# Optimization experiments

Hardware: AMD Instinct MI355X
Metric: run time of the kernel (lower is better)

Reference implementation:

```python
import jax, jax.numpy as jnp
import numpy as np

H = 48; W = 48; C_IN = 32; C_OUT = 64
L = 4                      # liftsamples
RADIUS = 3                 # neighborhood radius
CMCO = 16                  # LieConv PointConv fixed mid channels
FOCAL = W / np.pi          # equidistant fisheye focal
CX, CY = (W - 1) / 2.0, (H - 1) / 2.0
EPS = 1e-7


def _build_neighbor_indices(h, w, radius):
    offs = [(dx, dy) for dy in range(-radius, radius + 1)
            for dx in range(-radius, radius + 1)
            if dx * dx + dy * dy <= radius * radius]
    offs = np.array(offs, dtype=np.int64)  # (k,2) as (dx,dy)
    yy, xx = np.meshgrid(np.arange(h), np.arange(w), indexing='ij')
    yy = yy.reshape(-1, 1); xx = xx.reshape(-1, 1)
    ny = yy + offs[None, :, 1]; nx = xx + offs[None, :, 0]
    valid = (ny >= 0) & (ny < h) & (nx >= 0) & (nx < w)
    idx = ny * w + nx
    return np.where(valid, idx, -1).astype(np.int32)  # (h*w, k)


def swish(x):
    return x * jax.nn.sigmoid(x)


def so3_exp(wvec):
    # Rodrigues: (...,3) -> (...,3,3)
    th = jnp.maximum(jnp.linalg.norm(wvec, axis=-1, keepdims=True), EPS)
    k = wvec / th
    kx, ky, kz = k[..., 0], k[..., 1], k[..., 2]
    z = jnp.zeros_like(kx)
    K = jnp.stack([jnp.stack([z, -kz, ky], -1),
                   jnp.stack([kz, z, -kx], -1),
                   jnp.stack([-ky, kx, z], -1)], -2)
    th = th[..., None]
    I = jnp.eye(3, dtype=wvec.dtype)
    return I + jnp.sin(th) * K + (1.0 - jnp.cos(th)) * (K @ K)


def so3_log(R):
    # (...,3,3) -> (...,3)
    tr = R[..., 0, 0] + R[..., 1, 1] + R[..., 2, 2]
    cos = jnp.clip((tr - 1.0) * 0.5, -1.0 + 1e-6, 1.0 - 1e-6)
    th = jnp.arccos(cos)
    v = jnp.stack([R[..., 2, 1] - R[..., 1, 2],
                   R[..., 0, 2] - R[..., 2, 0],
                   R[..., 1, 0] - R[..., 0, 1]], -1)
    return v * (th / (2.0 * jnp.sin(th)))[..., None]


def setup_inputs() -> dict:
    key = jax.random.key(0)
    ks = jax.random.split(key, 6)
    def lin(k, fi, fo):
        return jax.random.normal(k, (fi, fo), jnp.float32) / np.sqrt(fi)
    return {
        'x': jax.random.normal(ks[0], (2, C_IN, H, W), jnp.float32),
        'neighbor_idx': jnp.asarray(_build_neighbor_indices(H, W, RADIUS)),
        'W1': lin(ks[1], 3, 32), 'b1': jnp.zeros((32,), jnp.float32),
        'W2': lin(ks[2], 32, 32), 'b2': jnp.zeros((32,), jnp.float32),
        'W3': lin(ks[3], 32, CMCO), 'b3': jnp.zeros((CMCO,), jnp.float32),
        'Wl': lin(ks[4], CMCO * C_IN, C_OUT), 'bl': jnp.zeros((C_OUT,), jnp.float32),
    }


def _lift_log(dtype):
    # pixel grid -> unit rays -> so(3) log of lifted group elems, shape (n*L, 3)
    u = jnp.arange(W, dtype=dtype); v = jnp.arange(H, dtype=dtype)
    uu, vv = jnp.meshgrid(u, v)               # 'xy' indexing, (H,W)
    dx = (uu - CX).reshape(-1); dy = (vv - CY).reshape(-1)
    r = jnp.sqrt(dx * dx + dy * dy)
    theta = r / FOCAL
    rs = jnp.maximum(r, EPS)
    rays = jnp.stack([jnp.sin(theta) * dx / rs,
                      jnp.sin(theta) * dy / rs,
                      jnp.cos(theta)], -1)    # (n,3)
    pz = jnp.clip(rays[:, 2], -1.0 + 1e-6, 1.0 - 1e-6)
    ang = jnp.arccos(pz)
    axis = jnp.stack([-rays[:, 1], rays[:, 0], jnp.zeros_like(pz)], -1)
    axis = axis / jnp.maximum(jnp.linalg.norm(axis, axis=-1, keepdims=True), EPS)
    Rp = so3_exp(axis * ang[:, None])          # (n,3,3), Rp @ e3 = ray
    alphas = jnp.arange(L, dtype=dtype) * (2.0 * np.pi / L)
    Rz = so3_exp(jnp.stack([jnp.zeros_like(alphas), jnp.zeros_like(alphas), alphas], -1))
    Rlift = jnp.einsum('nij,ljk->nlik', Rp, Rz)  # (n,L,3,3)
    return so3_log(Rlift).reshape(H * W * L, 3)


def reference(x, neighbor_idx, W1, b1, W2, b2, W3, b3, Wl, bl):
    bs, c, h, w = x.shape
    n = h * w
    k = neighbor_idx.shape[1]
    nL, K = n * L, k * L

    a = _lift_log(x.dtype)                                   # (nL,3)

    valid = neighbor_idx >= 0                                # (n,k)
    safe_pix = jnp.maximum(neighbor_idx, 0).astype(jnp.int32)
    # lifted neighbor indices: query lift copy l sees all (j, l') neighbors
    nb_lift = safe_pix[:, None, :, None] * L + jnp.arange(L, dtype=jnp.int32)[None, None, None, :]
    nb_lift = jnp.broadcast_to(nb_lift, (n, L, k, L)).reshape(nL, K)
    nb_pix = jnp.broadcast_to(safe_pix[:, None, :, None], (n, L, k, L)).reshape(nL, K)
    mask = jnp.broadcast_to(valid[:, None, :, None], (n, L, k, L)).reshape(nL, K)

    # pairwise group elements: log(exp(-b) @ exp(a))
    b_log = a[nb_lift]                                       # (nL,K,3)
    Rab = jnp.einsum('qmij,qjk->qmik', so3_exp(-b_log), so3_exp(a))
    ab = so3_log(Rab)                                        # (nL,K,3)

    # kernel MLP (WeightNet: 3 -> 32 -> 32 -> 16, swish)
    hdn = swish(ab @ W1 + b1)
    hdn = swish(hdn @ W2 + b2)
    wts = swish(hdn @ W3 + b3)                               # (nL,K,16)
    wts = jnp.where(mask[..., None], wts, 0.0)

    values = x.transpose(0, 2, 3, 1).reshape(bs, n, c)       # (bs,n,c)
    nv = values[:, nb_pix]                                   # (bs,nL,K,c)
    partial = jnp.einsum('bqmc,qmf->bqcf', nv, wts).reshape(bs, nL, c * CMCO)
    out = partial @ Wl + bl                                  # (bs,nL,c_out)
    out = out.reshape(bs, n, L, -1).mean(axis=2)             # pool over lift samples
    return out.reshape(bs, h, w, -1).transpose(0, 3, 1, 2)   # (bs,c_out,h,w)
```

## Files before the change

kernel.cpp:

```cpp
#include <hip/hip_runtime.h>

#define WW   48
#define NPIX 2304
#define CIN  32
#define COUT 64
#define KNB  29
#define FCO  16
#define NPJ  (NPIX * KNB)
#define GEN_WAVES  ((NPJ + 6) / 7)
#define GEN_BLOCKS ((GEN_WAVES + 3) / 4)

#define WS_RP64 0
#define WS_EAB  165888
#define WS_EG   248832
#define WS_M0   1133568
#define WS_V    1133632
#define WS_PART 4340800

__device__ __forceinline__ float swish_f(float x) {
    return x * __builtin_amdgcn_rcpf(1.0f + __expf(-x));
}

__device__ __forceinline__ void so3_exp_d(double wx, double wy, double wz, double R[9]) {
    double n  = sqrt(wx * wx + wy * wy + wz * wz);
    double th = fmax(n, 1e-7);
    double kx = wx / th, ky = wy / th, kz = wz / th;
    double s = sin(th), c = cos(th);
    double omc = 1.0 - c;
    R[0] = 1.0 + omc * (kx * kx - 1.0);
    R[1] = -s * kz + omc * kx * ky;
    R[2] =  s * ky + omc * kx * kz;
    R[3] =  s * kz + omc * kx * ky;
    R[4] = 1.0 + omc * (ky * ky - 1.0);
    R[5] = -s * kx + omc * ky * kz;
    R[6] = -s * ky + omc * kz * kx;
    R[7] =  s * kx + omc * kz * ky;
    R[8] = 1.0 + omc * (kz * kz - 1.0);
}

__device__ __forceinline__ void compute_Rp_d(int p, double R[9]) {
    int ui = p % WW, vi = p / WW;
    double dx = (double)ui - 23.5;
    double dy = (double)vi - 23.5;
    double r  = sqrt(dx * dx + dy * dy);
    const double FOCAL = 48.0 / 3.14159265358979323846;
    double theta = r / FOCAL;
    double rs = fmax(r, 1e-7);
    double st = sin(theta);
    double rayx = st * dx / rs;
    double rayy = st * dy / rs;
    double rayz = cos(theta);
    double pz  = fmin(fmax(rayz, -1.0 + 1e-6), 1.0 - 1e-6);
    double ang = acos(pz);
    double ax = -rayy, ay = rayx;
    double an = fmax(sqrt(ax * ax + ay * ay), 1e-7);
    ax /= an; ay /= an;
    so3_exp_d(ax * ang, ay * ang, 0.0, R);
}

__device__ __forceinline__ void mlp_half(float ab0, float ab1, float ab2, const int Q0,
    const float* __restrict__ W1, const float* __restrict__ b1,
    const float* __restrict__ W2, const float* __restrict__ b2,
    const float* __restrict__ W3, const float* __restrict__ b3,
    float* acc3) {
    float accq[16];
    #pragma unroll
    for (int q = 0; q < 16; ++q) accq[q] = b2[Q0 + q];
    #pragma unroll
    for (int i = 0; i < 32; ++i) {
        float h = swish_f(b1[i] + ab0 * W1[i] + ab1 * W1[32 + i] + ab2 * W1[64 + i]);
        #pragma unroll
        for (int q = 0; q < 16; ++q) accq[q] += h * W2[i * 32 + Q0 + q];
    }
    #pragma unroll
    for (int q = 0; q < 16; ++q) {
        float h2 = swish_f(accq[q]);
        #pragma unroll
        for (int f = 0; f < FCO; ++f) acc3[f] += h2 * W3[(Q0 + q) * FCO + f];
    }
}

__device__ __forceinline__ void mlp_eval(float ab0, float ab1, float ab2,
    const float* __restrict__ W1, const float* __restrict__ b1,
    const float* __restrict__ W2, const float* __restrict__ b2,
    const float* __restrict__ W3, const float* __restrict__ b3,
    float* o) {
    float acc3[FCO];
    #pragma unroll
    for (int f = 0; f < FCO; ++f) acc3[f] = b3[f];
    mlp_half(ab0, ab1, ab2, 0,  W1, b1, W2, b2, W3, b3, acc3);
    __builtin_amdgcn_sched_barrier(0);
    mlp_half(ab0, ab1, ab2, 16, W1, b1, W2, b2, W3, b3, acc3);
    #pragma unroll
    for (int f = 0; f < FCO; ++f) o[f] = swish_f(acc3[f]);
}

__global__ __launch_bounds__(256)
void rp_kernel(double* __restrict__ rp64, float* __restrict__ eab) {
    int p = blockIdx.x * 256 + threadIdx.x;
    if (p >= NPIX) return;
    double R[9];
    compute_Rp_d(p, R);
    #pragma unroll
    for (int e = 0; e < 9; ++e) rp64[p * 9 + e] = R[e];
    #pragma unroll
    for (int m = 0; m < 3; ++m) {
        int l = m + (m >> 1);
        double c = (l == 0) ? 1.0 : 0.0;
        double s = (l == 1) ? 1.0 : ((l == 3) ? -1.0 : 0.0);
        double M[9];
        #pragma unroll
        for (int i = 0; i < 3; ++i) {
            M[i * 3 + 0] =  R[i * 3 + 0] * c + R[i * 3 + 1] * s;
            M[i * 3 + 1] = -R[i * 3 + 0] * s + R[i * 3 + 1] * c;
            M[i * 3 + 2] =  R[i * 3 + 2];
        }
        double tr   = M[0] + M[4] + M[8];
        double cosv = fmin(fmax((tr - 1.0) * 0.5, -1.0 + 1e-6), 1.0 - 1e-6);
        double th   = acos(cosv);
        double sv   = sqrt((1.0 - cosv) * (1.0 + cosv));
        double fac  = th / (2.0 * sv);
        eab[p * 9 + m * 3 + 0] = (float)((M[7] - M[5]) * fac);
        eab[p * 9 + m * 3 + 1] = (float)((M[2] - M[6]) * fac);
        eab[p * 9 + m * 3 + 2] = (float)((M[3] - M[1]) * fac);
    }
}

__global__ __launch_bounds__(256)
void vlog2_kernel(const int* __restrict__ nbr, const double* __restrict__ rp64,
                  float* __restrict__ vws) {
    int tid = blockIdx.x * 256 + threadIdx.x;
    if (tid >= NPJ * 4) return;
    int g2 = tid >> 2;
    int d  = tid & 3;
    int p = g2 / KNB, j = g2 - p * KNB;
    int pj = max(nbr[p * KNB + j], 0);
    double Rq[9];
    #pragma unroll
    for (int q = 0; q < 9; ++q) Rq[q] = rp64[p * 9 + q];
    double X[9];
    #pragma unroll
    for (int q = 0; q < 9; ++q) X[q] = 0.0;
    #pragma unroll
    for (int k = 0; k < 3; ++k) {
        double rn0 = rp64[pj * 9 + k * 3 + 0];
        double rn1 = rp64[pj * 9 + k * 3 + 1];
        double rn2 = rp64[pj * 9 + k * 3 + 2];
        #pragma unroll
        for (int jj = 0; jj < 3; ++jj) {
            X[0 * 3 + jj] += rn0 * Rq[k * 3 + jj];
            X[1 * 3 + jj] += rn1 * Rq[k * 3 + jj];
            X[2 * 3 + jj] += rn2 * Rq[k * 3 + jj];
        }
    }
    double c = (d == 0) ? 1.0 : ((d == 2) ? -1.0 : 0.0);
    double s = (d == 1) ? 1.0 : ((d == 3) ? -1.0 : 0.0);
    double M0 =  X[0] * c + X[1] * s;
    double M1 = -X[0] * s + X[1] * c;
    double M2 =  X[2];
    double M3 =  X[3] * c + X[4] * s;
    double M4 = -X[3] * s + X[4] * c;
    double M5 =  X[5];
    double M6 =  X[6] * c + X[7] * s;
    double M7 = -X[6] * s + X[7] * c;
    double M8 =  X[8];
    double tr   = M0 + M4 + M8;
    double cosv = fmin(fmax((tr - 1.0) * 0.5, -1.0 + 1e-6), 1.0 - 1e-6);
    double th   = acos(cosv);
    double svv  = sqrt((1.0 - cosv) * (1.0 + cosv));
    double fac  = th / (2.0 * svv);
    float* dst = vws + g2 * 12 + d * 3;
    dst[0] = (float)((M7 - M5) * fac);
    dst[1] = (float)((M2 - M6) * fac);
    dst[2] = (float)((M3 - M1) * fac);
}

__global__ __launch_bounds__(256)
void edge_kernel(const float* __restrict__ W1, const float* __restrict__ b1,
                 const float* __restrict__ W2, const float* __restrict__ b2,
                 const float* __restrict__ W3, const float* __restrict__ b3,
                 const float* __restrict__ eab,
                 float* __restrict__ eg, float* __restrict__ m0v) {
    int g = blockIdx.x * 256 + threadIdx.x;
    if (g > NPIX * 6) return;
    bool isz = (g == NPIX * 6);
    int gc = isz ? 0 : g;
    int pix = gc / 6, which = gc - pix * 6;
    int m = (which < 3) ? which : (which - 3);
    float sg = isz ? 0.f : ((which < 3) ? 1.f : -1.f);
    const float* ep = eab + pix * 9 + m * 3;
    float o[FCO];
    mlp_eval(sg * ep[0], sg * ep[1], sg * ep[2], W1, b1, W2, b2, W3, b3, o);
    float* dst = isz ? m0v : (eg + g * FCO);
    #pragma unroll
    for (int f = 0; f < FCO; ++f) dst[f] = o[f];
}

__global__ __launch_bounds__(256)
void mlp1_kernel(const float* __restrict__ W1, const float* __restrict__ b1,
                 const float* __restrict__ W2, const float* __restrict__ b2,
                 const float* __restrict__ W3, const float* __restrict__ b3,
                 const float* __restrict__ vws, float* __restrict__ part) {
    int wave = blockIdx.x * 4 + (threadIdx.x >> 6);
    int lane = threadIdx.x & 63;
    int slot = lane / 9;
    int e    = lane - slot * 9;
    int g2   = wave * 7 + slot;
    int g2c  = min(g2, NPJ - 1);
    int l1m = e / 3, l2m = e - l1m * 3;
    int l1 = l1m + (l1m >> 1);
    int l2 = l2m + (l2m >> 1);
    int d  = (l1 - l2) & 3;
    const float* vp = vws + g2c * 12 + d * 3;
    float v0 = vp[0], v1 = vp[1], v2 = vp[2];
    float ab0 = (l2m == 0) ? v0 : ((l2m == 1) ?  v1 : -v1);
    float ab1 = (l2m == 0) ? v1 : ((l2m == 1) ? -v0 :  v0);
    float o[FCO];
    mlp_eval(ab0, ab1, v2, W1, b1, W2, b2, W3, b3, o);
    #pragma unroll
    for (int f = 0; f < FCO; ++f) {
        float a = o[f];
        a += __shfl(a, min(lane + 1, 63)) + __shfl(a, min(lane + 2, 63));
        a += __shfl(a, min(lane + 3, 63)) + __shfl(a, min(lane + 6, 63));
        o[f] = a;
    }
    if (e == 0 && lane < 63 && g2 < NPJ) {
        float* dst = part + g2 * FCO;
        #pragma unroll
        for (int f = 0; f < FCO; ++f) dst[f] = o[f];
    }
}

__global__ __launch_bounds__(256)
void agg_kernel(const float* __restrict__ x, const int* __restrict__ nbr,
                const float* __restrict__ Wl, const float* __restrict__ bl,
                const float* __restrict__ eg, const float* __restrict__ m0v,
                const float* __restrict__ part, float* __restrict__ out) {
    __shared__ int   spj[KNB];
    __shared__ int   sval[KNB];
    __shared__ float sE[FCO];
    __shared__ float sS[KNB][FCO];
    __shared__ float sxv[2][CIN][KNB];
    __shared__ float sT[2][CIN][FCO];
    __shared__ float spp[256];

    const int p = blockIdx.x;
    const int t = threadIdx.x;

    if (t < KNB) {
        int idx = nbr[p * KNB + t];
        spj[t]  = max(idx, 0);
        sval[t] = (idx >= 0) ? 1 : 0;
    } else if (t >= 32 && t < 32 + FCO) {
        int f = t - 32;
        sE[f] = eg[(p * 6 + 0) * FCO + f] + eg[(p * 6 + 1) * FCO + f]
              + eg[(p * 6 + 2) * FCO + f] + m0v[f];
    }
    __syncthreads();

    for (int e = t; e < 2 * CIN * KNB; e += 256) {
        int bb = e / (CIN * KNB);
        int r  = e - bb * (CIN * KNB);
        int c  = r / KNB;
        int j  = r - c * KNB;
        sxv[bb][c][j] = x[bb * (CIN * NPIX) + c * NPIX + spj[j]];
    }
    for (int idx = t; idx < KNB * FCO; idx += 256) {
        int j = idx >> 4, f = idx & 15;
        float acc = part[(p * KNB + j) * FCO + f];
        int n6 = spj[j] * 6;
        acc += eg[(n6 + 3) * FCO + f] + eg[(n6 + 4) * FCO + f] + eg[(n6 + 5) * FCO + f];
        acc += sE[f];
        sS[j][f] = sval[j] ? acc * 0.25f : 0.f;
    }
    __syncthreads();

    for (int tt = t; tt < 2 * CIN * FCO; tt += 256) {
        int bb = tt >> 9;
        int c  = (tt >> 4) & 31;
        int f  = tt & 15;
        float acc = 0.f;
        #pragma unroll
        for (int j = 0; j < KNB; ++j)
            acc += sxv[bb][c][j] * sS[j][f];
        sT[bb][c][f] = acc;
    }
    __syncthreads();

    {
        int half = t >> 7, q = t & 127, bb = q >> 6, co = q & 63;
        const float* Tb = &sT[bb][0][0];
        float acc = 0.f;
        int cf0 = half * 256;
        #pragma unroll 8
        for (int cf = cf0; cf < cf0 + 256; ++cf)
            acc += Tb[cf] * Wl[cf * COUT + co];
        spp[t] = acc;
    }
    __syncthreads();
    if (t < 128) {
        int bb = t >> 6, co = t & 63;
        out[bb * (COUT * NPIX) + co * NPIX + p] = spp[t] + spp[t + 128] + bl[co];
    }
}

extern "C" void kernel_launch(void* const* d_in, const int* in_sizes, int n_in,
                              void* d_out, int out_size, void* d_ws, size_t ws_size,
                              hipStream_t stream) {
    const float* x  = (const float*)d_in[0];
    const int* nbr  = (const int*)d_in[1];
    const float* W1 = (const float*)d_in[2];
    const float* b1 = (const float*)d_in[3];
    const float* W2 = (const float*)d_in[4];
    const float* b2 = (const float*)d_in[5];
    const float* W3 = (const float*)d_in[6];
    const float* b3 = (const float*)d_in[7];
    const float* Wl = (const float*)d_in[8];
    const float* bl = (const float*)d_in[9];
    float* out = (float*)d_out;

    char* ws = (char*)d_ws;
    double* rp64 = (double*)(ws + WS_RP64);
    float*  eab  = (float*)(ws + WS_EAB);
    float*  eg   = (float*)(ws + WS_EG);
    float*  m0v  = (float*)(ws + WS_M0);
    float*  vws  = (float*)(ws + WS_V);
    float*  part = (float*)(ws + WS_PART);

    hipLaunchKernelGGL(rp_kernel, dim3((NPIX + 255) / 256), dim3(256), 0, stream,
                       rp64, eab);
    hipLaunchKernelGGL(vlog2_kernel, dim3((NPJ * 4 + 255) / 256), dim3(256), 0, stream,
                       nbr, rp64, vws);
    hipLaunchKernelGGL(edge_kernel, dim3((NPIX * 6 + 1 + 255) / 256), dim3(256), 0, stream,
                       W1, b1, W2, b2, W3, b3, eab, eg, m0v);
    hipLaunchKernelGGL(mlp1_kernel, dim3(GEN_BLOCKS), dim3(256), 0, stream,
                       W1, b1, W2, b2, W3, b3, vws, part);
    hipLaunchKernelGGL(agg_kernel, dim3(NPIX), dim3(256), 0, stream,
                       x, nbr, Wl, bl, eg, m0v, part, out);
}
```

Measured before the change: 94.74 us.

## Split rp and edge MLP work across four threads and share Wl loads

rp_kernel now uses four threads per pixel, one writing the rotation and three computing the lifted logs, so more threads are in flight. edge_kernel splits each edge's MLP hidden layer across four lanes and combines the partial third-layer sums with xor shuffles, which cuts per-thread serial work and register pressure. In agg_kernel's final projection, 128 threads each load a Wl element once and apply it to both batches instead of 256 threads loading it separately. The cost is redundant compute of the pixel rotation and first layer in each lane, plus extra shuffles.

After: 86.29 us. 1.1x faster.

```diff
diff --git a/kernel.cpp b/kernel.cpp
--- a/kernel.cpp
+++ b/kernel.cpp
@@ -9,6 +9,7 @@
 #define NPJ  (NPIX * KNB)
 #define GEN_WAVES  ((NPJ + 6) / 7)
 #define GEN_BLOCKS ((GEN_WAVES + 3) / 4)
+#define NEDGE (NPIX * 6 + 1)
 
 #define WS_RP64 0
 #define WS_EAB  165888
@@ -97,14 +98,16 @@
 
 __global__ __launch_bounds__(256)
 void rp_kernel(double* __restrict__ rp64, float* __restrict__ eab) {
-    int p = blockIdx.x * 256 + threadIdx.x;
-    if (p >= NPIX) return;
+    int tid = blockIdx.x * 256 + threadIdx.x;
+    if (tid >= NPIX * 4) return;
+    int p = tid >> 2, which = tid & 3;
     double R[9];
     compute_Rp_d(p, R);
-    #pragma unroll
-    for (int e = 0; e < 9; ++e) rp64[p * 9 + e] = R[e];
-    #pragma unroll
-    for (int m = 0; m < 3; ++m) {
+    if (which == 0) {
+        #pragma unroll
+        for (int e = 0; e < 9; ++e) rp64[p * 9 + e] = R[e];
+    } else {
+        int m = which - 1;
         int l = m + (m >> 1);
         double c = (l == 0) ? 1.0 : 0.0;
         double s = (l == 1) ? 1.0 : ((l == 3) ? -1.0 : 0.0);
@@ -181,19 +184,48 @@
                  const float* __restrict__ W3, const float* __restrict__ b3,
                  const float* __restrict__ eab,
                  float* __restrict__ eg, float* __restrict__ m0v) {
-    int g = blockIdx.x * 256 + threadIdx.x;
-    if (g > NPIX * 6) return;
+    int tid = blockIdx.x * 256 + threadIdx.x;
+    int g  = tid >> 2;
+    int ql = tid & 3;
+    if (g >= NEDGE) return;
     bool isz = (g == NPIX * 6);
     int gc = isz ? 0 : g;
     int pix = gc / 6, which = gc - pix * 6;
     int m = (which < 3) ? which : (which - 3);
     float sg = isz ? 0.f : ((which < 3) ? 1.f : -1.f);
     const float* ep = eab + pix * 9 + m * 3;
-    float o[FCO];
-    mlp_eval(sg * ep[0], sg * ep[1], sg * ep[2], W1, b1, W2, b2, W3, b3, o);
-    float* dst = isz ? m0v : (eg + g * FCO);
-    #pragma unroll
-    for (int f = 0; f < FCO; ++f) dst[f] = o[f];
+    float ab0 = sg * ep[0], ab1 = sg * ep[1], ab2 = sg * ep[2];
+    const int Q0 = ql * 8;
+    float accq[8];
+    #pragma unroll
+    for (int q = 0; q < 8; ++q) accq[q] = b2[Q0 + q];
+    #pragma unroll
+    for (int i = 0; i < 32; ++i) {
+        float h = swish_f(b1[i] + ab0 * W1[i] + ab1 * W1[32 + i] + ab2 * W1[64 + i]);
+        #pragma unroll
+        for (int q = 0; q < 8; ++q) accq[q] += h * W2[i * 32 + Q0 + q];
+    }
+    float part3[FCO];
+    #pragma unroll
+    for (int f = 0; f < FCO; ++f) part3[f] = 0.f;
+    #pragma unroll
+    for (int q = 0; q < 8; ++q) {
+        float h2 = swish_f(accq[q]);
+        #pragma unroll
+        for (int f = 0; f < FCO; ++f) part3[f] += h2 * W3[(Q0 + q) * FCO + f];
+    }
+    #pragma unroll
+    for (int f = 0; f < FCO; ++f) {
+        float a = part3[f];
+        a += __shfl_xor(a, 1);
+        a += __shfl_xor(a, 2);
+        part3[f] = a;
+    }
+    if (ql == 0) {
+        float* dst = isz ? m0v : (eg + g * FCO);
+        #pragma unroll
+        for (int f = 0; f < FCO; ++f) dst[f] = swish_f(b3[f] + part3[f]);
+    }
 }
 
 __global__ __launch_bounds__(256)
@@ -287,20 +319,26 @@
     }
     __syncthreads();
 
-    {
-        int half = t >> 7, q = t & 127, bb = q >> 6, co = q & 63;
-        const float* Tb = &sT[bb][0][0];
-        float acc = 0.f;
+    if (t < 128) {
+        int half = t >> 6, co = t & 63;
+        const float* Tb0 = &sT[0][0][0];
+        const float* Tb1 = &sT[1][0][0];
+        float a0 = 0.f, a1 = 0.f;
         int cf0 = half * 256;
         #pragma unroll 8
-        for (int cf = cf0; cf < cf0 + 256; ++cf)
-            acc += Tb[cf] * Wl[cf * COUT + co];
-        spp[t] = acc;
+        for (int cf = cf0; cf < cf0 + 256; ++cf) {
+            float w = Wl[cf * COUT + co];
+            a0 += Tb0[cf] * w;
+            a1 += Tb1[cf] * w;
+        }
+        spp[half * 128 + 0 * 64 + co] = a0;
+        spp[half * 128 + 1 * 64 + co] = a1;
     }
     __syncthreads();
     if (t < 128) {
         int bb = t >> 6, co = t & 63;
-        out[bb * (COUT * NPIX) + co * NPIX + p] = spp[t] + spp[t + 128] + bl[co];
+        out[bb * (COUT * NPIX) + co * NPIX + p] =
+            spp[0 * 128 + bb * 64 + co] + spp[1 * 128 + bb * 64 + co] + bl[co];
     }
 }
 
@@ -327,11 +365,11 @@
     float*  vws  = (float*)(ws + WS_V);
     float*  part = (float*)(ws + WS_PART);
 
-    hipLaunchKernelGGL(rp_kernel, dim3((NPIX + 255) / 256), dim3(256), 0, stream,
+    hipLaunchKernelGGL(rp_kernel, dim3((NPIX * 4 + 255) / 256), dim3(256), 0, stream,
                        rp64, eab);
     hipLaunchKernelGGL(vlog2_kernel, dim3((NPJ * 4 + 255) / 256), dim3(256), 0, stream,
                        nbr, rp64, vws);
-    hipLaunchKernelGGL(edge_kernel, dim3((NPIX * 6 + 1 + 255) / 256), dim3(256), 0, stream,
+    hipLaunchKernelGGL(edge_kernel, dim3((NEDGE * 4 + 255) / 256), dim3(256), 0, stream,
                        W1, b1, W2, b2, W3, b3, eab, eg, m0v);
     hipLaunchKernelGGL(mlp1_kernel, dim3(GEN_BLOCKS), dim3(256), 0, stream,
                        W1, b1, W2, b2, W3, b3, vws, part);
```
